# Performance work log

Measured on AMD Instinct MI355X. Metric: run time of the kernel, lower is better.

Reference implementation:

```python
import jax, jax.numpy as jnp
import numpy as np

FEAT_STRIDE = 16
SCALES = np.array([8.0, 16.0, 32.0])
RATIOS = np.array([0.5, 1.0, 2.0])
PRE_NMS = 6000
POST_NMS = 300
NMS_THRESH = 0.7


def generate_anchors(base_size, ratios, scales):
    base = np.array([0.0, 0.0, base_size - 1.0, base_size - 1.0])

    def whctrs(a):
        w = a[2] - a[0] + 1.0
        h = a[3] - a[1] + 1.0
        return w, h, a[0] + 0.5 * (w - 1.0), a[1] + 0.5 * (h - 1.0)

    def mk(ws, hs, xc, yc):
        ws = ws[:, None]
        hs = hs[:, None]
        return np.hstack((xc - 0.5 * (ws - 1.0), yc - 0.5 * (hs - 1.0),
                          xc + 0.5 * (ws - 1.0), yc + 0.5 * (hs - 1.0)))

    w, h, xc, yc = whctrs(base)
    size = w * h
    size_ratios = size / ratios
    ws = np.round(np.sqrt(size_ratios))
    hs = np.round(ws * ratios)
    ratio_anchors = mk(ws, hs, xc, yc)
    out = []
    for a in ratio_anchors:
        w, h, xc, yc = whctrs(a)
        out.append(mk(w * scales, h * scales, xc, yc))
    return np.vstack(out).astype(np.float32)


def bbox_transform_inv(boxes, deltas):
    # boxes [..., 4], deltas [..., 4]
    w = boxes[..., 2] - boxes[..., 0] + 1.0
    h = boxes[..., 3] - boxes[..., 1] + 1.0
    cx = boxes[..., 0] + 0.5 * w
    cy = boxes[..., 1] + 0.5 * h
    pcx = deltas[..., 0] * w + cx
    pcy = deltas[..., 1] * h + cy
    pw = jnp.exp(deltas[..., 2]) * w
    ph = jnp.exp(deltas[..., 3]) * h
    return jnp.stack([pcx - 0.5 * pw, pcy - 0.5 * ph,
                      pcx + 0.5 * pw, pcy + 0.5 * ph], axis=-1)


def clip_boxes(boxes, im_info):
    # boxes [B, N, 4], im_info [B, 3] = (height, width, scale)
    hmax = (im_info[:, 0] - 1.0)[:, None]
    wmax = (im_info[:, 1] - 1.0)[:, None]
    x1 = jnp.clip(boxes[..., 0], 0.0, wmax)
    y1 = jnp.clip(boxes[..., 1], 0.0, hmax)
    x2 = jnp.clip(boxes[..., 2], 0.0, wmax)
    y2 = jnp.clip(boxes[..., 3], 0.0, hmax)
    return jnp.stack([x1, y1, x2, y2], axis=-1)


def nms_single(boxes, scores):
    # greedy NMS: boxes [M,4] already sorted desc by score, scores [M]
    M = boxes.shape[0]
    x1, y1, x2, y2 = boxes[:, 0], boxes[:, 1], boxes[:, 2], boxes[:, 3]
    areas = (x2 - x1 + 1.0) * (y2 - y1 + 1.0)
    idxs = jnp.arange(M)
    neg_inf = jnp.array(-jnp.inf, scores.dtype)

    def body(i, state):
        s, out = state
        j = jnp.argmax(s)
        valid = s[j] > neg_inf
        box = boxes[j]
        out = out.at[i].set(jnp.where(valid, box, jnp.zeros_like(box)))
        xx1 = jnp.maximum(box[0], x1)
        yy1 = jnp.maximum(box[1], y1)
        xx2 = jnp.minimum(box[2], x2)
        yy2 = jnp.minimum(box[3], y2)
        inter = jnp.maximum(0.0, xx2 - xx1 + 1.0) * jnp.maximum(0.0, yy2 - yy1 + 1.0)
        iou = inter / (areas[j] + areas - inter)
        sup = (iou > NMS_THRESH) | (idxs == j)
        s = jnp.where(valid & sup, neg_inf, s)
        return (s, out)

    out0 = jnp.zeros((POST_NMS, 4), boxes.dtype)
    _, out = jax.lax.fori_loop(0, POST_NMS, body, (scores, out0))
    return out


def setup_inputs() -> dict:
    key = jax.random.key(0)
    k1, k2 = jax.random.split(key)
    B, A, H, W = 16, 9, 100, 150
    scores = jax.random.normal(k1, (B, 2 * A, H, W), dtype=jnp.float32)
    bbox_deltas = 0.25 * jax.random.normal(k2, (B, 4 * A, H, W), dtype=jnp.float32)
    im_info = jnp.tile(jnp.array([[1600.0, 2400.0, 1.0]], dtype=jnp.float32), (B, 1))
    return {"scores": scores, "bbox_deltas": bbox_deltas, "im_info": im_info}


def reference(scores, bbox_deltas, im_info):
    B, C, H, W = scores.shape
    anchors_base = jnp.asarray(generate_anchors(FEAT_STRIDE, RATIOS, SCALES))
    A = anchors_base.shape[0]
    scores_fg = scores[:, A:, :, :]                       # [B, A, H, W]
    # anchor shifts over the feature grid
    sx, sy = jnp.meshgrid(jnp.arange(W) * FEAT_STRIDE, jnp.arange(H) * FEAT_STRIDE)
    shifts = jnp.stack([sx.ravel(), sy.ravel(), sx.ravel(), sy.ravel()], axis=1).astype(scores.dtype)  # [K,4]
    anchors = (anchors_base[None, :, :] + shifts[:, None, :]).reshape(-1, 4)  # [K*A, 4]
    deltas = bbox_deltas.transpose(0, 2, 3, 1).reshape(B, -1, 4)             # [B, K*A, 4]
    scr = scores_fg.transpose(0, 2, 3, 1).reshape(B, -1)                     # [B, K*A]
    proposals = bbox_transform_inv(anchors[None, :, :], deltas)
    proposals = clip_boxes(proposals, im_info)
    # sort desc, keep top pre_nms
    top_scores, order = jax.lax.top_k(scr, PRE_NMS)
    props_top = jnp.take_along_axis(proposals, order[..., None], axis=1)     # [B, PRE_NMS, 4]
    kept = jax.vmap(nms_single)(props_top, top_scores)                       # [B, POST_NMS, 4]
    batch_idx = jnp.broadcast_to(
        jnp.arange(B, dtype=scores.dtype)[:, None, None], (B, POST_NMS, 1))
    return jnp.concatenate([batch_idx, kept], axis=2)                        # [B, POST_NMS, 5]
```

## Files before the change

kernel.cpp:

```cpp
#include <hip/hip_runtime.h>
#include <cstdint>
#include <cmath>

#define HWSZ    15000
#define W_FEAT  150
#define A_NUM   9
#define NPER    135000
#define B_NUM   16
#define PRE_NMS 6000
#define POST_NMS 300
#define NBINS   16384
#define GCAP    2048
#define NGRP    6

__device__ __constant__ float ANC[9][4] = {
    {-84.f,  -40.f,  99.f,  55.f},
    {-176.f, -88.f, 191.f, 103.f},
    {-360.f,-184.f, 375.f, 199.f},
    {-56.f,  -56.f,  71.f,  71.f},
    {-120.f,-120.f, 135.f, 135.f},
    {-248.f,-248.f, 263.f, 263.f},
    {-36.f,  -80.f,  51.f,  95.f},
    {-80.f, -168.f,  95.f, 183.f},
    {-168.f,-344.f, 183.f, 359.f}};

__device__ __forceinline__ uint32_t fkey(float s) {
    uint32_t u = __float_as_uint(s);
    return (u & 0x80000000u) ? ~u : (u | 0x80000000u);
}

__device__ __forceinline__ bool iou_gt(const float4& q, float qa,
                                       const float4& c, float ca) {
    float xx1 = fmaxf(q.x, c.x);
    float yy1 = fmaxf(q.y, c.y);
    float xx2 = fminf(q.z, c.z);
    float yy2 = fminf(q.w, c.w);
    float iw = fmaxf(0.0f, __fadd_rn(__fsub_rn(xx2, xx1), 1.0f));
    float ih = fmaxf(0.0f, __fadd_rn(__fsub_rn(yy2, yy1), 1.0f));
    float inter = __fmul_rn(iw, ih);
    float den = __fsub_rn(__fadd_rn(qa, ca), inter);
    return (double)inter >= 0x1.666667p-1 * (double)den;
}

__device__ __forceinline__ float area_of(const float4& c) {
    return __fmul_rn(__fadd_rn(__fsub_rn(c.z, c.x), 1.0f),
                     __fadd_rn(__fsub_rn(c.w, c.y), 1.0f));
}

__global__ __launch_bounds__(1024) void k_hist(const float* __restrict__ scores,
                                               uint32_t* __restrict__ subhist) {
    __shared__ uint32_t hist[NBINS];
    int b = blockIdx.y, sx = blockIdx.x, S = gridDim.x, tid = threadIdx.x;
    for (int i = tid; i < NBINS; i += 1024) hist[i] = 0;
    __syncthreads();
    const float4* sc4 = (const float4*)(scores + (size_t)(b * 18 + 9) * HWSZ);
    int nf4 = NPER / 4;
    int per = (nf4 + S - 1) / S;
    int lo = sx * per, hi = min(lo + per, nf4);
    for (int i = lo + tid; i < hi; i += 1024) {
        float4 v = sc4[i];
        atomicAdd(&hist[fkey(v.x) >> 18], 1u);
        atomicAdd(&hist[fkey(v.y) >> 18], 1u);
        atomicAdd(&hist[fkey(v.z) >> 18], 1u);
        atomicAdd(&hist[fkey(v.w) >> 18], 1u);
    }
    __syncthreads();
    uint32_t* out = subhist + ((size_t)b * S + sx) * NBINS;
    for (int i = tid; i < NBINS; i += 1024) out[i] = hist[i];
}

__global__ __launch_bounds__(1024) void k_scan(const uint32_t* __restrict__ subhist,
                                               int S, uint32_t* __restrict__ scum,
                                               uint32_t* __restrict__ gbase) {
    __shared__ uint32_t tl[NBINS];
    __shared__ uint32_t psum[1024];
    __shared__ uint32_t gb[8];
    int b = blockIdx.x, tid = threadIdx.x;
    for (int i = tid; i < NBINS; i += 1024) {
        uint32_t t = 0;
        for (int u = 0; u < S; ++u) t += subhist[((size_t)b * S + u) * NBINS + i];
        tl[i] = t;
    }
    if (tid < 8) gb[tid] = 0xFFFFFFFFu;
    __syncthreads();
    int base = NBINS - 16 * (tid + 1);
    uint32_t csum = 0;
#pragma unroll
    for (int i = 0; i < 16; ++i) csum += tl[base + i];
    psum[tid] = csum;
    __syncthreads();
    for (int off = 1; off < 1024; off <<= 1) {
        uint32_t v = (tid >= off) ? psum[tid - off] : 0u;
        __syncthreads();
        psum[tid] += v;
        __syncthreads();
    }
    uint32_t c = tid ? psum[tid - 1] : 0u;
    for (int i = 15; i >= 0; --i) {
        uint32_t t = tl[base + i];
        scum[(size_t)b * NBINS + base + i] = c;
        if (t && c < PRE_NMS) atomicMin(&gb[c >> 10], c);
        c += t;
    }
    __syncthreads();
    if (tid < 8) gbase[b * 8 + tid] = gb[tid];
}

__global__ __launch_bounds__(1024) void k_compact(
        const float* __restrict__ scores, const uint32_t* __restrict__ scum,
        uint64_t* __restrict__ cand, uint32_t* __restrict__ gcnt) {
    __shared__ uint32_t sl[NBINS];
    __shared__ uint32_t lc[NGRP], lb[NGRP];
    int b = blockIdx.y, sx = blockIdx.x, S = gridDim.x, tid = threadIdx.x;
    for (int i = tid; i < NBINS; i += 1024) sl[i] = scum[(size_t)b * NBINS + i];
    if (tid < NGRP) lc[tid] = 0;
    __syncthreads();
    const float4* sc4 = (const float4*)(scores + (size_t)(b * 18 + 9) * HWSZ);
    int nf4 = NPER / 4;
    int per = (nf4 + S - 1) / S;
    int lo = sx * per, hi = min(lo + per, nf4);
    for (int i0 = lo; i0 < hi; i0 += 1024) {
        int i = i0 + tid;
        bool w[4];
        uint32_t gg[4], pp[4];
        uint64_t rec[4];
#pragma unroll
        for (int c = 0; c < 4; ++c) w[c] = false;
        if (i < hi) {
            float4 v = sc4[i];
            float cc[4] = {v.x, v.y, v.z, v.w};
#pragma unroll
            for (int c = 0; c < 4; ++c) {
                uint32_t k = fkey(cc[c]);
                uint32_t sc = sl[k >> 18];
                if (sc < PRE_NMS) {
                    w[c] = true;
                    gg[c] = sc >> 10;
                    pp[c] = atomicAdd(&lc[gg[c]], 1u);
                    int e = 4 * i + c;
                    int a = e / HWSZ, p = e - a * HWSZ;
                    rec[c] = ((uint64_t)(~k) << 32) | (uint32_t)(p * A_NUM + a);
                }
            }
        }
        __syncthreads();
        if (tid < NGRP && lc[tid])
            lb[tid] = atomicAdd(&gcnt[(b * NGRP + tid) * 16], lc[tid]);
        __syncthreads();
#pragma unroll
        for (int c = 0; c < 4; ++c)
            if (w[c]) {
                uint32_t pos = lb[gg[c]] + pp[c];
                if (pos < GCAP)
                    cand[((size_t)b * NGRP + gg[c]) * GCAP + pos] = rec[c];
            }
        __syncthreads();
        if (tid < NGRP) lc[tid] = 0;
        __syncthreads();
    }
}

__global__ __launch_bounds__(1024) void k_group(
        const uint64_t* __restrict__ cand, const uint32_t* __restrict__ gcnt,
        const float* __restrict__ deltas, const float* __restrict__ im_info,
        const uint32_t* __restrict__ gbase, float4* __restrict__ boxes) {
    __shared__ uint64_t s[GCAP];
    int b = blockIdx.y, g = blockIdx.x, tid = threadIdx.x;
    uint32_t base = gbase[b * 8 + g];
    if (base == 0xFFFFFFFFu) return;
    uint32_t cnt = min(gcnt[(b * NGRP + g) * 16], (uint32_t)GCAP);
    for (int i = tid; i < GCAP; i += 1024)
        s[i] = (i < (int)cnt) ? cand[((size_t)b * NGRP + g) * GCAP + i] : ~0ull;
    __syncthreads();
    for (unsigned k = 2; k <= GCAP; k <<= 1) {
        for (unsigned j = k >> 1; j; j >>= 1) {
            unsigned p = tid;
            unsigned i = ((p & ~(j - 1)) << 1) | (p & (j - 1));
            unsigned ixj = i | j;
            uint64_t x = s[i], y = s[ixj];
            bool up = ((i & k) == 0);
            if (up ? (x > y) : (x < y)) { s[i] = y; s[ixj] = x; }
            __syncthreads();
        }
    }
    float him = im_info[b * 3 + 0], wim = im_info[b * 3 + 1];
    float ymax = __fsub_rn(him, 1.0f), xmax = __fsub_rn(wim, 1.0f);
    for (int r = tid; r < GCAP; r += 1024) {
        uint32_t P = base + (uint32_t)r;
        uint32_t idx = (uint32_t)s[r];
        if (r < (int)cnt && P < PRE_NMS && idx < NPER) {
            int a = idx % A_NUM;
            int p = idx / A_NUM;
            int wc = p % W_FEAT, hr = p / W_FEAT;
            float ax1 = ANC[a][0] + (float)(wc * 16);
            float ay1 = ANC[a][1] + (float)(hr * 16);
            float ax2 = ANC[a][2] + (float)(wc * 16);
            float ay2 = ANC[a][3] + (float)(hr * 16);
            const float* dp = deltas + (size_t)(b * 36 + a * 4) * HWSZ + p;
            float dx = dp[0], dy = dp[HWSZ], dw = dp[2 * HWSZ], dh = dp[3 * HWSZ];
            float ww = __fadd_rn(__fsub_rn(ax2, ax1), 1.0f);
            float hh = __fadd_rn(__fsub_rn(ay2, ay1), 1.0f);
            float cx = __fadd_rn(ax1, __fmul_rn(0.5f, ww));
            float cy = __fadd_rn(ay1, __fmul_rn(0.5f, hh));
            float pcx = __fadd_rn(__fmul_rn(dx, ww), cx);
            float pcy = __fadd_rn(__fmul_rn(dy, hh), cy);
            float ew = (float)exp((double)dw);
            float eh = (float)exp((double)dh);
            float pw = __fmul_rn(ew, ww);
            float ph = __fmul_rn(eh, hh);
            float x1 = __fsub_rn(pcx, __fmul_rn(0.5f, pw));
            float y1 = __fsub_rn(pcy, __fmul_rn(0.5f, ph));
            float x2 = __fadd_rn(pcx, __fmul_rn(0.5f, pw));
            float y2 = __fadd_rn(pcy, __fmul_rn(0.5f, ph));
            float4 bx;
            bx.x = fminf(fmaxf(x1, 0.0f), xmax);
            bx.y = fminf(fmaxf(y1, 0.0f), ymax);
            bx.z = fminf(fmaxf(x2, 0.0f), xmax);
            bx.w = fminf(fmaxf(y2, 0.0f), ymax);
            boxes[(size_t)b * PRE_NMS + P] = bx;
        }
    }
}

__global__ __launch_bounds__(256) void k_mask(const float4* __restrict__ boxes,
                                              uint64_t* __restrict__ masks,
                                              int NC, int NW, int T) {
    int b = blockIdx.y;
    int wv = threadIdx.x >> 6, lane = threadIdx.x & 63;
    int t = blockIdx.x * 4 + wv;
    if (t >= T) return;
    int ti = 0, rem = t;
    while (rem >= NW - ti) { rem -= NW - ti; ++ti; }
    int tj = ti + rem;
    __shared__ float4 colb[4][64];
    __shared__ float  cola[4][64];
    const float4* bb = boxes + (size_t)b * PRE_NMS;
    int i = ti * 64 + lane;
    float4 c = bb[i];
    float ca = area_of(c);
    float4 q0 = bb[tj * 64 + lane];
    colb[wv][lane] = q0;
    cola[wv][lane] = area_of(q0);
    asm volatile("s_waitcnt lgkmcnt(0)" ::: "memory");
    __builtin_amdgcn_wave_barrier();
    uint64_t m = 0;
    if (ti == tj) {
#pragma unroll
        for (int jj = 0; jj < 64; ++jj) {
            bool hit = (jj > lane) && iou_gt(colb[wv][jj], cola[wv][jj], c, ca);
            m |= ((uint64_t)(hit ? 1u : 0u)) << jj;
        }
    } else {
#pragma unroll
        for (int jj = 0; jj < 64; ++jj) {
            bool hit = iou_gt(colb[wv][jj], cola[wv][jj], c, ca);
            m |= ((uint64_t)(hit ? 1u : 0u)) << jj;
        }
    }
    masks[((size_t)b * NW + tj) * NC + i] = m;
}

#define PROC(P)                                                                \
    do {                                                                       \
        float ca = area_of(P);                                                 \
        bool viol = false;                                                     \
        if (K > 0)   viol |= (lane       < K) & iou_gt(k0, a0, P, ca);         \
        if (K > 64)  viol |= (lane + 64  < K) & iou_gt(k1, a1, P, ca);         \
        if (K > 128) viol |= (lane + 128 < K) & iou_gt(k2, a2, P, ca);         \
        if (K > 192) viol |= (lane + 192 < K) & iou_gt(k3, a3, P, ca);         \
        if (K > 256) viol |= (lane + 256 < K) & iou_gt(k4, a4, P, ca);         \
        if (!__any((int)viol)) {                                               \
            int sl = K >> 6, tg = K & 63;                                      \
            if (lane == tg) {                                                  \
                switch (sl) {                                                  \
                case 0: k0 = P; a0 = ca; break;                                \
                case 1: k1 = P; a1 = ca; break;                                \
                case 2: k2 = P; a2 = ca; break;                                \
                case 3: k3 = P; a3 = ca; break;                                \
                default: k4 = P; a4 = ca; break;                               \
                }                                                              \
            }                                                                  \
            ++K;                                                               \
        }                                                                      \
    } while (0)

#define RSTEP(RG)                                                              \
    do {                                                                       \
        if (!fin && i < NC) {                                                  \
            bool mine = (lane == (i >> 6));                                    \
            bool sb = mine && ((sup >> (i & 63)) & 1ull);                      \
            if (!__any((int)sb)) {                                             \
                int sl = K >> 6, tg = K & 63;                                  \
                if (lane == tg) {                                              \
                    switch (sl) {                                              \
                    case 0: i0 = i; break;                                     \
                    case 1: i1 = i; break;                                     \
                    case 2: i2 = i; break;                                     \
                    case 3: i3 = i; break;                                     \
                    default: i4 = i; break;                                    \
                    }                                                          \
                }                                                              \
                if (lane < NW) sup |= RG;                                      \
                ++K;                                                           \
                if (K >= POST_NMS) fin = true;                                 \
            }                                                                  \
            int nx = i + 8; if (nx >= NC) nx = NC - 1;                         \
            RG = mrow[nx];                                                     \
            ++i;                                                               \
        }                                                                      \
    } while (0)

__global__ __launch_bounds__(64) void k_resolve(const float4* __restrict__ boxes,
                                                const uint64_t* __restrict__ masks,
                                                int NC, int NW,
                                                float* __restrict__ out) {
    int b = blockIdx.x, lane = threadIdx.x;
    const float4* bb = boxes + (size_t)b * PRE_NMS;
    int K = 0;
    int i0 = 0, i1 = 0, i2 = 0, i3 = 0, i4 = 0;
    bool fin = false;

    if (NC > 0) {
        const uint64_t* mrow =
            masks + ((size_t)b * NW + (lane < NW ? lane : NW - 1)) * NC;
        uint64_t sup = 0;
        uint64_t r0 = mrow[0], r1 = mrow[1], r2 = mrow[2], r3 = mrow[3];
        uint64_t r4 = mrow[4], r5 = mrow[5], r6 = mrow[6], r7 = mrow[7];
        int i = 0;
        while (i < NC && !fin) {
            RSTEP(r0); RSTEP(r1); RSTEP(r2); RSTEP(r3);
            RSTEP(r4); RSTEP(r5); RSTEP(r6); RSTEP(r7);
        }
    }

    float4 k0, k1, k2, k3, k4;
    float a0, a1, a2, a3, a4;
    { int id = (lane       < K) ? i0 : 0; k0 = bb[id]; a0 = area_of(k0); }
    { int id = (lane + 64  < K) ? i1 : 0; k1 = bb[id]; a1 = area_of(k1); }
    { int id = (lane + 128 < K) ? i2 : 0; k2 = bb[id]; a2 = area_of(k2); }
    { int id = (lane + 192 < K) ? i3 : 0; k3 = bb[id]; a3 = area_of(k3); }
    { int id = (lane + 256 < K) ? i4 : 0; k4 = bb[id]; a4 = area_of(k4); }

    if (!fin && NC < PRE_NMS) {
        float4 p0 = bb[NC + 0], p1 = bb[NC + 1], p2 = bb[NC + 2], p3 = bb[NC + 3];
        bool done = false;
        for (int r = NC; r < PRE_NMS && !done; r += 4) {
            int n = r + 4;
            float4 n0 = bb[(n + 0 < PRE_NMS) ? n + 0 : PRE_NMS - 1];
            float4 n1 = bb[(n + 1 < PRE_NMS) ? n + 1 : PRE_NMS - 1];
            float4 n2 = bb[(n + 2 < PRE_NMS) ? n + 2 : PRE_NMS - 1];
            float4 n3 = bb[(n + 3 < PRE_NMS) ? n + 3 : PRE_NMS - 1];
            PROC(p0); if (K >= POST_NMS) done = true;
            if (!done) { PROC(p1); if (K >= POST_NMS) done = true; }
            if (!done) { PROC(p2); if (K >= POST_NMS) done = true; }
            if (!done) { PROC(p3); if (K >= POST_NMS) done = true; }
            p0 = n0; p1 = n1; p2 = n2; p3 = n3;
        }
    }

#pragma unroll
    for (int s = 0; s < 5; ++s) {
        int idx = s * 64 + lane;
        if (idx < POST_NMS) {
            float4 c;
            switch (s) {
            case 0: c = k0; break;
            case 1: c = k1; break;
            case 2: c = k2; break;
            case 3: c = k3; break;
            default: c = k4; break;
            }
            bool v = idx < K;
            float* o = out + (size_t)(b * POST_NMS + idx) * 5;
            o[0] = (float)b;
            o[1] = v ? c.x : 0.f;
            o[2] = v ? c.y : 0.f;
            o[3] = v ? c.z : 0.f;
            o[4] = v ? c.w : 0.f;
        }
    }
}

extern "C" void kernel_launch(void* const* d_in, const int* in_sizes, int n_in,
                              void* d_out, int out_size, void* d_ws, size_t ws_size,
                              hipStream_t stream) {
    const float* scores  = (const float*)d_in[0];
    const float* deltas  = (const float*)d_in[1];
    const float* im_info = (const float*)d_in[2];
    float* out = (float*)d_out;
    char* ws = (char*)d_ws;

    const size_t boxB   = (size_t)B_NUM * PRE_NMS * 16;
    const size_t scumB  = (size_t)B_NUM * NBINS * 4;
    const size_t metaB  = 8192;
    const size_t candB  = (size_t)B_NUM * NGRP * GCAP * 8;
    const size_t fixedB = boxB + scumB + metaB;
    int NC = 0, S = 1;
    const int lad[2] = {2048, 1024};
    for (int li = 0; li < 2 && !NC; ++li) {
        size_t mb = 2ull * lad[li] * lad[li];
        if (fixedB + 1048576ull + candB + mb <= ws_size) {
            NC = lad[li];
            for (int ss = 8; ss >= 1; ss >>= 1)
                if (fixedB + (size_t)ss * 1048576ull + candB + mb <= ws_size) { S = ss; break; }
        }
    }
    if (!NC) { NC = 1024; S = 1; }
    int NW = NC / 64;

    float4*   boxes   = (float4*)ws;
    uint32_t* scum    = (uint32_t*)(ws + boxB);
    uint32_t* gbase   = (uint32_t*)(ws + boxB + scumB);
    uint32_t* gcnt    = (uint32_t*)(ws + boxB + scumB + 1024);
    uint32_t* subhist = (uint32_t*)(ws + fixedB);
    uint64_t* cand    = (uint64_t*)(ws + fixedB + (size_t)S * 1048576ull);
    uint64_t* masks   = (uint64_t*)(ws + fixedB + (size_t)S * 1048576ull + candB);

    hipMemsetAsync(gcnt, 0, (size_t)B_NUM * NGRP * 16 * 4, stream);

    dim3 gh(S, B_NUM);
    k_hist<<<gh, 1024, 0, stream>>>(scores, subhist);
    k_scan<<<B_NUM, 1024, 0, stream>>>(subhist, S, scum, gbase);
    k_compact<<<gh, 1024, 0, stream>>>(scores, scum, cand, gcnt);
    dim3 gg(NGRP, B_NUM);
    k_group<<<gg, 1024, 0, stream>>>(cand, gcnt, deltas, im_info, gbase, boxes);
    int T = NW * (NW + 1) / 2;
    dim3 gm((T + 3) / 4, B_NUM);
    k_mask<<<gm, 256, 0, stream>>>(boxes, masks, NC, NW, T);
    k_resolve<<<B_NUM, 64, 0, stream>>>(boxes, masks, NC, NW, out);
}
```

Before: 162.0 us.

## Resolve NMS masks word-by-word with kept-row OR and fold gcnt reset into scan

The serial per-candidate resolve loop, which ran one wave vote per candidate, becomes a per-64-candidate word loop. For each word, the mask words of already-kept boxes are gathered and OR-reduced across the wave by shuffles, and the survivors within the word are then picked greedily using the diagonal mask broadcast by shuffle. The separate hipMemsetAsync of gcnt is removed, and the counters are zeroed inside k_scan, which saves one launch. The new loop trades sequential per-candidate latency for gathered loads from up to 300 kept rows per word.

Measured after the change: 186.5 us. 1.15x slower.

```diff
diff --git a/kernel.cpp b/kernel.cpp
--- a/kernel.cpp
+++ b/kernel.cpp
@@ -71,7 +71,8 @@
 
 __global__ __launch_bounds__(1024) void k_scan(const uint32_t* __restrict__ subhist,
                                                int S, uint32_t* __restrict__ scum,
-                                               uint32_t* __restrict__ gbase) {
+                                               uint32_t* __restrict__ gbase,
+                                               uint32_t* __restrict__ gcnt) {
     __shared__ uint32_t tl[NBINS];
     __shared__ uint32_t psum[1024];
     __shared__ uint32_t gb[8];
@@ -82,6 +83,7 @@
         tl[i] = t;
     }
     if (tid < 8) gb[tid] = 0xFFFFFFFFu;
+    if (tid < NGRP) gcnt[(b * NGRP + tid) * 16] = 0;
     __syncthreads();
     int base = NBINS - 16 * (tid + 1);
     uint32_t csum = 0;
@@ -284,52 +286,48 @@
         }                                                                      \
     } while (0)
 
-#define RSTEP(RG)                                                              \
-    do {                                                                       \
-        if (!fin && i < NC) {                                                  \
-            bool mine = (lane == (i >> 6));                                    \
-            bool sb = mine && ((sup >> (i & 63)) & 1ull);                      \
-            if (!__any((int)sb)) {                                             \
-                int sl = K >> 6, tg = K & 63;                                  \
-                if (lane == tg) {                                              \
-                    switch (sl) {                                              \
-                    case 0: i0 = i; break;                                     \
-                    case 1: i1 = i; break;                                     \
-                    case 2: i2 = i; break;                                     \
-                    case 3: i3 = i; break;                                     \
-                    default: i4 = i; break;                                    \
-                    }                                                          \
-                }                                                              \
-                if (lane < NW) sup |= RG;                                      \
-                ++K;                                                           \
-                if (K >= POST_NMS) fin = true;                                 \
-            }                                                                  \
-            int nx = i + 8; if (nx >= NC) nx = NC - 1;                         \
-            RG = mrow[nx];                                                     \
-            ++i;                                                               \
-        }                                                                      \
-    } while (0)
-
 __global__ __launch_bounds__(64) void k_resolve(const float4* __restrict__ boxes,
                                                 const uint64_t* __restrict__ masks,
                                                 int NC, int NW,
                                                 float* __restrict__ out) {
     int b = blockIdx.x, lane = threadIdx.x;
     const float4* bb = boxes + (size_t)b * PRE_NMS;
+    const uint64_t* mk = masks + (size_t)b * NW * NC;
     int K = 0;
     int i0 = 0, i1 = 0, i2 = 0, i3 = 0, i4 = 0;
     bool fin = false;
 
-    if (NC > 0) {
-        const uint64_t* mrow =
-            masks + ((size_t)b * NW + (lane < NW ? lane : NW - 1)) * NC;
-        uint64_t sup = 0;
-        uint64_t r0 = mrow[0], r1 = mrow[1], r2 = mrow[2], r3 = mrow[3];
-        uint64_t r4 = mrow[4], r5 = mrow[5], r6 = mrow[6], r7 = mrow[7];
-        int i = 0;
-        while (i < NC && !fin) {
-            RSTEP(r0); RSTEP(r1); RSTEP(r2); RSTEP(r3);
-            RSTEP(r4); RSTEP(r5); RSTEP(r6); RSTEP(r7);
+    for (int w = 0; w < NW && !fin; ++w) {
+        const uint64_t* mw = mk + (size_t)w * NC;
+        uint64_t d = mw[(w << 6) + lane];
+        uint64_t acc = 0;
+        if (lane       < K) acc |= mw[i0];
+        if (lane + 64  < K) acc |= mw[i1];
+        if (lane + 128 < K) acc |= mw[i2];
+        if (lane + 192 < K) acc |= mw[i3];
+        if (lane + 256 < K) acc |= mw[i4];
+#pragma unroll
+        for (int off = 1; off < 64; off <<= 1)
+            acc |= (uint64_t)__shfl_xor((unsigned long long)acc, off);
+        uint64_t avail = ~acc;
+        while (avail && !fin) {
+            int j0 = __ffsll((unsigned long long)avail) - 1;
+            int idx = (w << 6) + j0;
+            int sl = K >> 6, tg = K & 63;
+            if (lane == tg) {
+                switch (sl) {
+                case 0: i0 = idx; break;
+                case 1: i1 = idx; break;
+                case 2: i2 = idx; break;
+                case 3: i3 = idx; break;
+                default: i4 = idx; break;
+                }
+            }
+            ++K;
+            if (K >= POST_NMS) { fin = true; break; }
+            uint64_t dj = (uint64_t)__shfl((unsigned long long)d, j0);
+            avail &= ~dj;
+            avail &= ~(1ull << j0);
         }
     }
 
@@ -416,11 +414,9 @@
     uint64_t* cand    = (uint64_t*)(ws + fixedB + (size_t)S * 1048576ull);
     uint64_t* masks   = (uint64_t*)(ws + fixedB + (size_t)S * 1048576ull + candB);
 
-    hipMemsetAsync(gcnt, 0, (size_t)B_NUM * NGRP * 16 * 4, stream);
-
     dim3 gh(S, B_NUM);
     k_hist<<<gh, 1024, 0, stream>>>(scores, subhist);
-    k_scan<<<B_NUM, 1024, 0, stream>>>(subhist, S, scum, gbase);
+    k_scan<<<B_NUM, 1024, 0, stream>>>(subhist, S, scum, gbase, gcnt);
     k_compact<<<gh, 1024, 0, stream>>>(scores, scum, cand, gcnt);
     dim3 gg(NGRP, B_NUM);
     k_group<<<gg, 1024, 0, stream>>>(cand, gcnt, deltas, im_info, gbase, boxes);
```
